# Performance work log

Measured on AMD Instinct MI355X. Metric: run time of the kernel, lower is better.

The kernel has to match this reference:

```python
import jax, jax.numpy as jnp
import numpy as np

DECAY = 0.8
COMMITMENT = 1.0
EPS = 1e-05


def setup_inputs() -> dict:
    key = jax.random.key(0)
    k1, k2 = jax.random.split(key)
    x = jax.random.normal(k1, (8, 4096, 256), dtype=jnp.float32)
    embed = jax.random.normal(k2, (8192, 256), dtype=jnp.float32)
    cluster_size = jnp.zeros((8192,), dtype=jnp.float32)
    embed_avg = embed  # torch registers embed_avg = embed.clone()
    return {"x": x, "embed": embed, "cluster_size": cluster_size, "embed_avg": embed_avg}


def reference(x, embed, cluster_size, embed_avg):
    # EuclideanCodebook.forward (training mode) + VectorQuantize straight-through.
    K, D = embed.shape
    shape = x.shape
    flatten = x.reshape(-1, D)  # [T, D], T = B*N

    dist = (2.0 * (flatten @ embed.T)
            - jnp.sum(flatten * flatten, axis=-1, keepdims=True)
            - jnp.sum(embed * embed, axis=-1)[None, :])  # [T, K]
    embed_ind = jnp.argmax(dist, axis=-1)  # [T]

    quantize = embed[embed_ind].reshape(shape)  # gather

    # EMA codebook statistics (scatter-add instead of materializing one-hot [T,K])
    bins = jax.ops.segment_sum(jnp.ones_like(embed_ind, dtype=x.dtype), embed_ind, num_segments=K)  # [K]
    embed_sum = jax.ops.segment_sum(flatten, embed_ind, num_segments=K)  # [K, D]

    new_cluster_size = cluster_size * DECAY + (1.0 - DECAY) * bins
    new_embed_avg = embed_avg * DECAY + (1.0 - DECAY) * embed_sum

    total = new_cluster_size.sum()
    smoothed = (new_cluster_size + EPS) / (total + K * EPS) * total  # laplace smoothing
    new_embed = new_embed_avg / smoothed[:, None]

    commit_loss = jnp.mean((jax.lax.stop_gradient(quantize) - x) ** 2) * COMMITMENT
    quantize_st = x + jax.lax.stop_gradient(quantize - x)  # straight-through

    ind_out = embed_ind.reshape(shape[:-1])
    return quantize_st, ind_out, commit_loss, new_embed, new_cluster_size, new_embed_avg
```

## Files before the change

kernel.cpp:

```cpp
#include <hip/hip_runtime.h>

#define DECAYF 0.8f
#define OMDF   0.2f
#define EPSF   1e-5f
#define COMMITF 1.0f
#define MARGINF 0.024f
#define FIXCAP  8192
#define MAXR    64

typedef _Float16 h8v __attribute__((ext_vector_type(8)));
typedef float f4v __attribute__((ext_vector_type(4)));

__device__ inline void gload_lds16(const void* g, void* l) {
  __builtin_amdgcn_global_load_lds(
      (const __attribute__((address_space(1))) unsigned int*)g,
      (__attribute__((address_space(3))) unsigned int*)l, 16, 0, 0);
}

__global__ __launch_bounds__(256) void k_pre(
    const float* __restrict__ embed, char* __restrict__ Ews,
    float* __restrict__ zero_p, int zero_n, float* __restrict__ ee, int K, int D)
{
  const int tid = threadIdx.x;
  const int gid0 = blockIdx.x * 256 + tid;
  const int gstride = gridDim.x * 256;

  for (int i = gid0; i < zero_n; i += gstride) zero_p[i] = 0.0f;

  for (int gid = gid0; gid < K * (D / 8); gid += gstride) {
    int k = gid >> 5;
    int d0 = (gid & 31) * 8;
    const float* ep = embed + (size_t)k * D + d0;
    float4 v0 = *(const float4*)(ep);
    float4 v1 = *(const float4*)(ep + 4);
    float f[8] = {v0.x, v0.y, v0.z, v0.w, v1.x, v1.y, v1.z, v1.w};
    h8v h;
#pragma unroll
    for (int e = 0; e < 8; ++e) h[e] = (_Float16)f[e];
    int tt = k >> 6;
    int c = k & 63;
    int byteoff = c * 512 + ((d0 * 2) ^ ((c & 7) << 4));
    *(h8v*)(Ews + (size_t)tt * 32768 + byteoff) = h;
  }

  {
    int wave = tid >> 6;
    int lane = tid & 63;
    int k = blockIdx.x * 4 + wave;
    if (k < K) {
      const float* e = embed + (size_t)k * D;
      float s = 0.f;
      for (int d = lane * 4; d < D; d += 256) {
        float4 v = *reinterpret_cast<const float4*>(e + d);
        s += v.x * v.x + v.y * v.y + v.z * v.z + v.w * v.w;
      }
      for (int off = 32; off > 0; off >>= 1) s += __shfl_down(s, off);
      if (lane == 0) ee[k] = 0.5f * s;
    }
  }
}

__device__ __forceinline__ void upd2(float s, int code, float& b1, float& b2, int& bi) {
  if (s > b1) { b2 = b1; b1 = s; bi = code; }
  else if (s > b2) { b2 = s; }
}

__device__ __forceinline__ void k_body(
    int TT, int NT, char* lds, const char* Ews, const float* ee,
    int w, int lane, int l15, int rowbyte0,
    const int (&dbyte)[8],
    const h8v (&xh)[4][8],
    f4v (&CUR)[4], f4v (&PRV)[4],
    float EEP, float& EEC,
    float (&best)[4][4], float (&bst2)[4][4], int (&bidx)[4][4])
{
  const int k0 = TT * 64;
  const char* cb = lds + (TT & 1) * 32768;
  if (TT + 1 < NT) {
    const char* src = Ews + (size_t)(TT + 1) * 32768 + w * 8192 + lane * 16;
    char* dst = lds + ((TT + 1) & 1) * 32768 + w * 8192;
#pragma unroll
    for (int q = 0; q < 8; ++q) gload_lds16(src + q * 1024, dst + q * 1024);
  }
  EEC = ee[k0 + w * 16 + l15];
  const int cp = k0 - 64 + w * 16 + l15;
#pragma unroll
  for (int rf = 0; rf < 4; ++rf) CUR[rf] = (f4v){0.f, 0.f, 0.f, 0.f};
  h8v B[2];
  B[0] = *(const h8v*)(cb + rowbyte0 + dbyte[0]);
#pragma unroll
  for (int ks = 0; ks < 8; ++ks) {
    const int cs = ks & 1, ns = cs ^ 1;
    if (ks < 7) B[ns] = *(const h8v*)(cb + rowbyte0 + dbyte[ks + 1]);
    __builtin_amdgcn_s_setprio(1);
    CUR[0] = __builtin_amdgcn_mfma_f32_16x16x32_f16(xh[0][ks], B[cs], CUR[0], 0, 0, 0);
    CUR[1] = __builtin_amdgcn_mfma_f32_16x16x32_f16(xh[1][ks], B[cs], CUR[1], 0, 0, 0);
    CUR[2] = __builtin_amdgcn_mfma_f32_16x16x32_f16(xh[2][ks], B[cs], CUR[2], 0, 0, 0);
    CUR[3] = __builtin_amdgcn_mfma_f32_16x16x32_f16(xh[3][ks], B[cs], CUR[3], 0, 0, 0);
    __builtin_amdgcn_s_setprio(0);
    {
      const int s0 = 2 * ks, s1 = 2 * ks + 1;
      const int rf0 = s0 >> 2, ii0 = s0 & 3;
      const int rf1 = s1 >> 2, ii1 = s1 & 3;
      upd2(PRV[rf0][ii0] - EEP, cp, best[rf0][ii0], bst2[rf0][ii0], bidx[rf0][ii0]);
      upd2(PRV[rf1][ii1] - EEP, cp, best[rf1][ii1], bst2[rf1][ii1], bidx[rf1][ii1]);
    }
  }
  __syncthreads();
}

__global__ __launch_bounds__(256, 2) void k_dist(
    const float* __restrict__ x, const char* __restrict__ Ews,
    const float* __restrict__ ee, float* __restrict__ ind_f,
    int* __restrict__ idx_out, int* __restrict__ wl, int* __restrict__ cnt,
    int T, int K)
{
  extern __shared__ char lds[];
  const int tid = threadIdx.x;
  const int w = tid >> 6, lane = tid & 63;
  const int l15 = lane & 15, lk = lane >> 4;
  const int row0 = blockIdx.x * 64;
  const int NT = K / 64;

  h8v xh[4][8];
#pragma unroll
  for (int rf = 0; rf < 4; ++rf) {
    const float* xp = x + (size_t)(row0 + rf * 16 + l15) * 256 + lk * 8;
#pragma unroll
    for (int ks = 0; ks < 8; ++ks) {
      float4 v0 = *(const float4*)(xp + ks * 32);
      float4 v1 = *(const float4*)(xp + ks * 32 + 4);
      float f[8] = {v0.x, v0.y, v0.z, v0.w, v1.x, v1.y, v1.z, v1.w};
      h8v h;
#pragma unroll
      for (int e = 0; e < 8; ++e) h[e] = (_Float16)f[e];
      xh[rf][ks] = h;
    }
  }

  float best[4][4], bst2[4][4];
  int bidx[4][4];
#pragma unroll
  for (int rf = 0; rf < 4; ++rf)
#pragma unroll
    for (int i = 0; i < 4; ++i) { best[rf][i] = -3.0e38f; bst2[rf][i] = -3.0e38f; bidx[rf][i] = 0; }

  const int swz = (l15 & 7) << 4;
  const int rowbyte0 = (w * 16 + l15) * 512;
  int dbyte[8];
#pragma unroll
  for (int ks = 0; ks < 8; ++ks) dbyte[ks] = (ks * 64 + lk * 16) ^ swz;

  {
    const char* src = Ews + (size_t)w * 8192 + lane * 16;
    char* dst = lds + w * 8192;
#pragma unroll
    for (int q = 0; q < 8; ++q)
      gload_lds16(src + q * 1024, dst + q * 1024);
  }
  __syncthreads();

  f4v accA[4], accB[4];
#pragma unroll
  for (int rf = 0; rf < 4; ++rf)
    accB[rf] = (f4v){-3.0e38f, -3.0e38f, -3.0e38f, -3.0e38f};
  float eeX = 0.f, eeY = 0.f;

  for (int tt = 0; tt < NT; tt += 2) {
    k_body(tt,     NT, lds, Ews, ee, w, lane, l15, rowbyte0, dbyte, xh,
           accA, accB, eeX, eeY, best, bst2, bidx);
    k_body(tt + 1, NT, lds, Ews, ee, w, lane, l15, rowbyte0, dbyte, xh,
           accB, accA, eeY, eeX, best, bst2, bidx);
  }
  {
    const int cp = (NT - 1) * 64 + w * 16 + l15;
#pragma unroll
    for (int rf = 0; rf < 4; ++rf)
#pragma unroll
      for (int ii = 0; ii < 4; ++ii)
        upd2(accB[rf][ii] - eeX, cp, best[rf][ii], bst2[rf][ii], bidx[rf][ii]);
  }

#pragma unroll
  for (int rf = 0; rf < 4; ++rf)
#pragma unroll
    for (int i = 0; i < 4; ++i) {
      float s = best[rf][i], s2 = bst2[rf][i];
      int mi = bidx[rf][i];
#pragma unroll
      for (int off = 1; off < 16; off <<= 1) {
        float os = __shfl_xor(s, off);
        float os2 = __shfl_xor(s2, off);
        int oi = __shfl_xor(mi, off);
        if (os > s || (os == s && oi < mi)) {
          s2 = fmaxf(s, os2);
          s = os; mi = oi;
        } else {
          s2 = fmaxf(s2, os);
        }
      }
      best[rf][i] = s; bst2[rf][i] = s2; bidx[rf][i] = mi;
    }

  float* S  = (float*)lds;
  float* S2 = S + 256;
  int*   MI = (int*)(S2 + 256);
  if (l15 == 0) {
#pragma unroll
    for (int rf = 0; rf < 4; ++rf)
#pragma unroll
      for (int i = 0; i < 4; ++i) {
        int rl = rf * 16 + lk * 4 + i;
        int a = w * 64 + rl;
        S[a]  = best[rf][i];
        S2[a] = bst2[rf][i];
        MI[a] = bidx[rf][i];
      }
  }
  __syncthreads();
  if (w == 0) {
    int r = lane;
    float s = S[r], s2 = S2[r];
    int mi = MI[r];
#pragma unroll
    for (int q = 1; q < 4; ++q) {
      float sq = S[q * 64 + r], s2q = S2[q * 64 + r];
      int miq = MI[q * 64 + r];
      if (sq > s) { s2 = fmaxf(s, s2q); s = sq; mi = miq; }
      else        { s2 = fmaxf(s2, sq); }
    }
    int row = row0 + r;
    idx_out[row] = mi;
    ind_f[row] = (float)mi;
    if (s - s2 < MARGINF) {
      int slot = atomicAdd(cnt, 1);
      if (slot < FIXCAP) wl[slot] = row;
    }
  }
}

__global__ __launch_bounds__(256) void k_fix1(
    const float* __restrict__ x, const float* __restrict__ embed,
    const float* __restrict__ ee, const int* __restrict__ wl,
    const int* __restrict__ cnt, float* __restrict__ pval,
    int* __restrict__ pidx)
{
  __shared__ float Xs[8][256];
  const int b = blockIdx.x & 255;
  const int g = blockIdx.x >> 8;
  const int t = threadIdx.x;
  int n = *cnt; if (n > FIXCAP) n = FIXCAP;
  const int c = b * 32 + (t & 31);
  const float* er = embed + (size_t)c * 256;
  const float eec = ee[c];
  const int rl = t >> 5;

  for (int r0 = g * 8; r0 < n; r0 += 32) {
    __syncthreads();
    for (int i = t; i < 8 * 64; i += 256) {
      int rr = i >> 6, dq = i & 63;
      int wi = r0 + rr; if (wi >= n) wi = n - 1;
      int row = wl[wi];
      ((float4*)Xs[rr])[dq] = *(const float4*)(x + (size_t)row * 256 + dq * 4);
    }
    __syncthreads();
    const float* xr = Xs[rl];
    float s0 = 0.f, s1 = 0.f, s2a = 0.f, s3 = 0.f;
#pragma unroll
    for (int d = 0; d < 256; d += 16) {
      float4 e0 = *(const float4*)(er + d);
      float4 e1 = *(const float4*)(er + d + 4);
      float4 e2 = *(const float4*)(er + d + 8);
      float4 e3 = *(const float4*)(er + d + 12);
      s0 = fmaf(xr[d + 0], e0.x, s0);  s0 = fmaf(xr[d + 1], e0.y, s0);
      s0 = fmaf(xr[d + 2], e0.z, s0);  s0 = fmaf(xr[d + 3], e0.w, s0);
      s1 = fmaf(xr[d + 4], e1.x, s1);  s1 = fmaf(xr[d + 5], e1.y, s1);
      s1 = fmaf(xr[d + 6], e1.z, s1);  s1 = fmaf(xr[d + 7], e1.w, s1);
      s2a = fmaf(xr[d + 8], e2.x, s2a);  s2a = fmaf(xr[d + 9], e2.y, s2a);
      s2a = fmaf(xr[d + 10], e2.z, s2a); s2a = fmaf(xr[d + 11], e2.w, s2a);
      s3 = fmaf(xr[d + 12], e3.x, s3);  s3 = fmaf(xr[d + 13], e3.y, s3);
      s3 = fmaf(xr[d + 14], e3.z, s3);  s3 = fmaf(xr[d + 15], e3.w, s3);
    }
    float s = ((s0 + s1) + (s2a + s3)) - eec;
    int mi = c;
#pragma unroll
    for (int off = 1; off < 32; off <<= 1) {
      float os = __shfl_xor(s, off);
      int oi = __shfl_xor(mi, off);
      if (os > s || (os == s && oi < mi)) { s = os; mi = oi; }
    }
    int wi = r0 + rl;
    if ((t & 31) == 0 && wi < n) {
      pval[(size_t)wi * 256 + b] = s;
      pidx[(size_t)wi * 256 + b] = mi;
    }
  }
}

__global__ __launch_bounds__(256) void k_fix2(
    const int* __restrict__ wl, const int* __restrict__ cnt,
    const float* __restrict__ pval, const int* __restrict__ pidx,
    float* __restrict__ ind_f, int* __restrict__ idx_out)
{
  __shared__ float bv[256];
  __shared__ int bi[256];
  const int t = threadIdx.x;
  int n = *cnt; if (n > FIXCAP) n = FIXCAP;
  for (int it = blockIdx.x; it < n; it += gridDim.x) {
    __syncthreads();
    bv[t] = pval[(size_t)it * 256 + t];
    bi[t] = pidx[(size_t)it * 256 + t];
    __syncthreads();
    for (int sh = 128; sh > 0; sh >>= 1) {
      if (t < sh) {
        if (bv[t + sh] > bv[t] || (bv[t + sh] == bv[t] && bi[t + sh] < bi[t])) {
          bv[t] = bv[t + sh]; bi[t] = bi[t + sh];
        }
      }
      __syncthreads();
    }
    if (t == 0) {
      int row = wl[it];
      idx_out[row] = bi[0];
      ind_f[row] = (float)bi[0];
    }
  }
}

__global__ __launch_bounds__(256) void k_cnt(
    const int* __restrict__ idx, int* __restrict__ cntr, int* __restrict__ rlist,
    int* __restrict__ olist, int* __restrict__ ocnt, int T)
{
  int r = blockIdx.x * 256 + threadIdx.x;
  if (r >= T) return;
  int k = idx[r];
  int slot = atomicAdd(&cntr[k], 1);
  if (slot < MAXR) rlist[k * MAXR + slot] = r;
  else { int o = atomicAdd(ocnt, 1); olist[o] = r; }
}

__global__ __launch_bounds__(256) void k_ovf(
    const float* __restrict__ x, const int* __restrict__ idx,
    const int* __restrict__ olist, const int* __restrict__ ocnt,
    float* __restrict__ ovfsum)
{
  int wave = threadIdx.x >> 6, lane = threadIdx.x & 63;
  int n = *ocnt;
  for (int i = blockIdx.x * 4 + wave; i < n; i += gridDim.x * 4) {
    int row = olist[i];
    int k = idx[row];
    int d0 = lane * 4;
    float4 xv = *(const float4*)(x + (size_t)row * 256 + d0);
    atomicAdd(&ovfsum[(size_t)k * 256 + d0 + 0], xv.x);
    atomicAdd(&ovfsum[(size_t)k * 256 + d0 + 1], xv.y);
    atomicAdd(&ovfsum[(size_t)k * 256 + d0 + 2], xv.z);
    atomicAdd(&ovfsum[(size_t)k * 256 + d0 + 3], xv.w);
  }
}

__global__ void k_gather(const float* __restrict__ x, const float* __restrict__ embed,
                         const int* __restrict__ idx, float* __restrict__ quant,
                         float* __restrict__ lslots, int T, int D)
{
  int wave = threadIdx.x >> 6;
  int lane = threadIdx.x & 63;
  int row = blockIdx.x * 4 + wave;
  if (row >= T) return;
  int k = idx[row];
  const float* xr = x + (size_t)row * D;
  const float* er = embed + (size_t)k * D;
  float* qr = quant + (size_t)row * D;
  float lsum = 0.f;
  for (int d = lane * 4; d < D; d += 256) {
    float4 xv = *reinterpret_cast<const float4*>(xr + d);
    float4 ev = *reinterpret_cast<const float4*>(er + d);
    *reinterpret_cast<float4*>(qr + d) = ev;
    float dx = ev.x - xv.x, dy = ev.y - xv.y, dz = ev.z - xv.z, dw = ev.w - xv.w;
    lsum += dx * dx + dy * dy + dz * dz + dw * dw;
  }
  for (int off = 32; off > 0; off >>= 1) lsum += __shfl_down(lsum, off);
  if (lane == 0) atomicAdd(&lslots[row & 255], lsum);
}

__global__ void k_ema1(const float* __restrict__ cs, const int* __restrict__ cntr,
                       float* __restrict__ ncs, float* __restrict__ total_acc, int K)
{
  int k = blockIdx.x * 256 + threadIdx.x;
  float v = 0.f;
  if (k < K) {
    v = cs[k] * DECAYF + OMDF * (float)cntr[k];
    ncs[k] = v;
  }
  for (int off = 32; off > 0; off >>= 1) v += __shfl_down(v, off);
  __shared__ float s4[4];
  if ((threadIdx.x & 63) == 0) s4[threadIdx.x >> 6] = v;
  __syncthreads();
  if (threadIdx.x == 0) atomicAdd(total_acc, s4[0] + s4[1] + s4[2] + s4[3]);
}

__global__ __launch_bounds__(256) void k_ema2(
    const float* __restrict__ x, const float* __restrict__ ea,
    const int* __restrict__ cntr, const int* __restrict__ rlist,
    const float* __restrict__ ovfsum, const float* __restrict__ ncs,
    const float* __restrict__ total_acc, float* __restrict__ ne,
    float* __restrict__ nea, int K, int D)
{
  int wave = threadIdx.x >> 6, lane = threadIdx.x & 63;
  int k = blockIdx.x * 4 + wave;
  if (k >= K) return;
  int c = cntr[k];
  int m = c < MAXR ? c : MAXR;
  int d0 = lane * 4;
  float4 s = *(const float4*)(ovfsum + (size_t)k * 256 + d0);
  for (int i = 0; i < m; ++i) {
    int r = rlist[k * MAXR + i];
    float4 xv = *(const float4*)(x + (size_t)r * 256 + d0);
    s.x += xv.x; s.y += xv.y; s.z += xv.z; s.w += xv.w;
  }
  float4 eav = *(const float4*)(ea + (size_t)k * 256 + d0);
  float total = *total_acc;
  float csk = ncs[k];
  float sm = (csk + EPSF) / (total + (float)K * EPSF) * total;
  float rs = 1.0f / sm;
  float v0 = eav.x * DECAYF + OMDF * s.x;
  float v1 = eav.y * DECAYF + OMDF * s.y;
  float v2 = eav.z * DECAYF + OMDF * s.z;
  float v3 = eav.w * DECAYF + OMDF * s.w;
  size_t o = (size_t)k * 256 + d0;
  nea[o + 0] = v0; nea[o + 1] = v1; nea[o + 2] = v2; nea[o + 3] = v3;
  ne[o + 0] = v0 * rs; ne[o + 1] = v1 * rs; ne[o + 2] = v2 * rs; ne[o + 3] = v3 * rs;
}

__global__ void k_loss(const float* __restrict__ lslots, float* __restrict__ out_loss,
                       float scale)
{
  int tid = threadIdx.x;
  float v = lslots[tid];
  for (int off = 32; off > 0; off >>= 1) v += __shfl_down(v, off);
  __shared__ float s4[4];
  if ((tid & 63) == 0) s4[tid >> 6] = v;
  __syncthreads();
  if (tid == 0) out_loss[0] = (s4[0] + s4[1] + s4[2] + s4[3]) * scale;
}

extern "C" void kernel_launch(void* const* d_in, const int* in_sizes, int n_in,
                              void* d_out, int out_size, void* d_ws, size_t ws_size,
                              hipStream_t stream)
{
  const float* x     = (const float*)d_in[0];
  const float* embed = (const float*)d_in[1];
  const float* cs    = (const float*)d_in[2];
  const float* ea    = (const float*)d_in[3];
  const int K = in_sizes[2];
  const int D = in_sizes[1] / K;
  const int T = in_sizes[0] / D;

  float* out   = (float*)d_out;
  float* o_q   = out;
  float* o_ind = out + (size_t)T * D;
  float* o_ls  = o_ind + T;
  float* o_ne  = o_ls + 1;
  float* o_ncs = o_ne + (size_t)K * D;
  float* o_nea = o_ncs + K;

  float* w      = (float*)d_ws;
  float* ee     = w;
  int*   idx    = (int*)(w + K);
  int*   wl     = idx + T;
  float* pval   = (float*)(wl + FIXCAP);
  int*   pidx   = (int*)(pval + (size_t)FIXCAP * 256);
  int*   rlist  = pidx + (size_t)FIXCAP * 256;
  int*   olist  = rlist + (size_t)K * MAXR;
  float* ovfsum = (float*)(olist + T);
  float* lslots = ovfsum + (size_t)K * D;
  float* total  = lslots + 256;
  int*   cnt    = (int*)(total + 1);
  int*   cntr   = cnt + 1;
  int*   ocnt   = cntr + K;
  int zero_n = K * D + 256 + 1 + 1 + K + 1;
  size_t ews_off = (((size_t)(ocnt + 1 - (int*)w)) + 63) & ~(size_t)63;
  char* Ews = (char*)(w + ews_off);

  k_pre<<<2048, 256, 0, stream>>>(embed, Ews, ovfsum, zero_n, ee, K, D);
  k_dist<<<T / 64, 256, 65536, stream>>>(x, Ews, ee, o_ind, idx, wl, cnt, T, K);
  k_fix1<<<1024, 256, 0, stream>>>(x, embed, ee, wl, cnt, pval, pidx);
  k_fix2<<<1024, 256, 0, stream>>>(wl, cnt, pval, pidx, o_ind, idx);
  k_cnt<<<(T + 255) / 256, 256, 0, stream>>>(idx, cntr, rlist, olist, ocnt, T);
  k_ovf<<<128, 256, 0, stream>>>(x, idx, olist, ocnt, ovfsum);
  k_gather<<<(T + 3) / 4, 256, 0, stream>>>(x, embed, idx, o_q, lslots, T, D);
  k_ema1<<<(K + 255) / 256, 256, 0, stream>>>(cs, cntr, o_ncs, total, K);
  k_ema2<<<(K + 3) / 4, 256, 0, stream>>>(x, ea, cntr, rlist, ovfsum, o_ncs, total,
                                          o_ne, o_nea, K, D);
  k_loss<<<1, 256, 0, stream>>>(lslots, o_ls, COMMITF / ((float)T * (float)D));
}
```

Measured before the change: 476.7 us.

## Fuse gather, loss and bin counting into distance and fix kernels

Moves the codeword gather, commitment-loss accumulation and per-code row-list bucketing into the tail of the distance kernel for rows that are confidently assigned. Rows flagged for exact re-check are handled the same way at the end of the fix2 kernel once their final index is known. This drops two separate kernel launches and a re-read of the index array. In exchange the distance kernel gets a longer serial epilogue with atomics, and the LDS allocation becomes static.

```diff
diff --git a/kernel.cpp b/kernel.cpp
--- a/kernel.cpp
+++ b/kernel.cpp
@@ -111,11 +111,15 @@
 
 __global__ __launch_bounds__(256, 2) void k_dist(
     const float* __restrict__ x, const char* __restrict__ Ews,
-    const float* __restrict__ ee, float* __restrict__ ind_f,
-    int* __restrict__ idx_out, int* __restrict__ wl, int* __restrict__ cnt,
+    const float* __restrict__ ee, const float* __restrict__ embed,
+    float* __restrict__ ind_f, int* __restrict__ idx_out,
+    int* __restrict__ wl, int* __restrict__ cnt,
+    float* __restrict__ quant, float* __restrict__ lslots,
+    int* __restrict__ cntr, int* __restrict__ rlist,
+    int* __restrict__ olist, int* __restrict__ ocnt,
     int T, int K)
 {
-  extern __shared__ char lds[];
+  __shared__ char lds[65536];
   const int tid = threadIdx.x;
   const int w = tid >> 6, lane = tid & 63;
   const int l15 = lane & 15, lk = lane >> 4;
@@ -205,6 +209,8 @@
   float* S  = (float*)lds;
   float* S2 = S + 256;
   int*   MI = (int*)(S2 + 256);
+  int*   FK = MI + 256;
+  int*   FF = FK + 64;
   if (l15 == 0) {
 #pragma unroll
     for (int rf = 0; rf < 4; ++rf)
@@ -232,9 +238,31 @@
     int row = row0 + r;
     idx_out[row] = mi;
     ind_f[row] = (float)mi;
+    int flagged = 0;
     if (s - s2 < MARGINF) {
       int slot = atomicAdd(cnt, 1);
-      if (slot < FIXCAP) wl[slot] = row;
+      if (slot < FIXCAP) { wl[slot] = row; flagged = 1; }
+    }
+    FK[r] = mi;
+    FF[r] = flagged;
+  }
+  __syncthreads();
+
+  for (int rr = w * 16; rr < w * 16 + 16; ++rr) {
+    if (FF[rr]) continue;
+    const int row = row0 + rr;
+    const int k = FK[rr];
+    const float4 xv = *(const float4*)(x + (size_t)row * 256 + lane * 4);
+    const float4 ev = *(const float4*)(embed + (size_t)k * 256 + lane * 4);
+    *(float4*)(quant + (size_t)row * 256 + lane * 4) = ev;
+    float dx = ev.x - xv.x, dy = ev.y - xv.y, dz = ev.z - xv.z, dw = ev.w - xv.w;
+    float l = dx * dx + dy * dy + dz * dz + dw * dw;
+    for (int off = 32; off > 0; off >>= 1) l += __shfl_down(l, off);
+    if (lane == 0) {
+      atomicAdd(&lslots[row & 255], l);
+      int slot = atomicAdd(&cntr[k], 1);
+      if (slot < MAXR) rlist[k * MAXR + slot] = row;
+      else { int o = atomicAdd(ocnt, 1); olist[o] = row; }
     }
   }
 }
@@ -298,9 +326,13 @@
 }
 
 __global__ __launch_bounds__(256) void k_fix2(
+    const float* __restrict__ x, const float* __restrict__ embed,
     const int* __restrict__ wl, const int* __restrict__ cnt,
     const float* __restrict__ pval, const int* __restrict__ pidx,
-    float* __restrict__ ind_f, int* __restrict__ idx_out)
+    float* __restrict__ ind_f, int* __restrict__ idx_out,
+    float* __restrict__ quant, float* __restrict__ lslots,
+    int* __restrict__ cntr, int* __restrict__ rlist,
+    int* __restrict__ olist, int* __restrict__ ocnt)
 {
   __shared__ float bv[256];
   __shared__ int bi[256];
@@ -319,24 +351,28 @@
       }
       __syncthreads();
     }
+    const int row = wl[it];
+    const int kf = bi[0];
     if (t == 0) {
-      int row = wl[it];
-      idx_out[row] = bi[0];
-      ind_f[row] = (float)bi[0];
-    }
-  }
-}
-
-__global__ __launch_bounds__(256) void k_cnt(
-    const int* __restrict__ idx, int* __restrict__ cntr, int* __restrict__ rlist,
-    int* __restrict__ olist, int* __restrict__ ocnt, int T)
-{
-  int r = blockIdx.x * 256 + threadIdx.x;
-  if (r >= T) return;
-  int k = idx[r];
-  int slot = atomicAdd(&cntr[k], 1);
-  if (slot < MAXR) rlist[k * MAXR + slot] = r;
-  else { int o = atomicAdd(ocnt, 1); olist[o] = r; }
+      idx_out[row] = kf;
+      ind_f[row] = (float)kf;
+      int slot = atomicAdd(&cntr[kf], 1);
+      if (slot < MAXR) rlist[kf * MAXR + slot] = row;
+      else { int o = atomicAdd(ocnt, 1); olist[o] = row; }
+    }
+    float xv = x[(size_t)row * 256 + t];
+    float ev = embed[(size_t)kf * 256 + t];
+    quant[(size_t)row * 256 + t] = ev;
+    float d = ev - xv;
+    __syncthreads();
+    bv[t] = d * d;
+    __syncthreads();
+    for (int sh = 128; sh > 0; sh >>= 1) {
+      if (t < sh) bv[t] += bv[t + sh];
+      __syncthreads();
+    }
+    if (t == 0) atomicAdd(&lslots[row & 255], bv[0]);
+  }
 }
 
 __global__ __launch_bounds__(256) void k_ovf(
@@ -356,30 +392,6 @@
     atomicAdd(&ovfsum[(size_t)k * 256 + d0 + 2], xv.z);
     atomicAdd(&ovfsum[(size_t)k * 256 + d0 + 3], xv.w);
   }
-}
-
-__global__ void k_gather(const float* __restrict__ x, const float* __restrict__ embed,
-                         const int* __restrict__ idx, float* __restrict__ quant,
-                         float* __restrict__ lslots, int T, int D)
-{
-  int wave = threadIdx.x >> 6;
-  int lane = threadIdx.x & 63;
-  int row = blockIdx.x * 4 + wave;
-  if (row >= T) return;
-  int k = idx[row];
-  const float* xr = x + (size_t)row * D;
-  const float* er = embed + (size_t)k * D;
-  float* qr = quant + (size_t)row * D;
-  float lsum = 0.f;
-  for (int d = lane * 4; d < D; d += 256) {
-    float4 xv = *reinterpret_cast<const float4*>(xr + d);
-    float4 ev = *reinterpret_cast<const float4*>(er + d);
-    *reinterpret_cast<float4*>(qr + d) = ev;
-    float dx = ev.x - xv.x, dy = ev.y - xv.y, dz = ev.z - xv.z, dw = ev.w - xv.w;
-    lsum += dx * dx + dy * dy + dz * dz + dw * dw;
-  }
-  for (int off = 32; off > 0; off >>= 1) lsum += __shfl_down(lsum, off);
-  if (lane == 0) atomicAdd(&lslots[row & 255], lsum);
 }
 
 __global__ void k_ema1(const float* __restrict__ cs, const int* __restrict__ cntr,
@@ -482,12 +494,12 @@
   char* Ews = (char*)(w + ews_off);
 
   k_pre<<<2048, 256, 0, stream>>>(embed, Ews, ovfsum, zero_n, ee, K, D);
-  k_dist<<<T / 64, 256, 65536, stream>>>(x, Ews, ee, o_ind, idx, wl, cnt, T, K);
+  k_dist<<<T / 64, 256, 0, stream>>>(x, Ews, ee, embed, o_ind, idx, wl, cnt,
+                                     o_q, lslots, cntr, rlist, olist, ocnt, T, K);
   k_fix1<<<1024, 256, 0, stream>>>(x, embed, ee, wl, cnt, pval, pidx);
-  k_fix2<<<1024, 256, 0, stream>>>(wl, cnt, pval, pidx, o_ind, idx);
-  k_cnt<<<(T + 255) / 256, 256, 0, stream>>>(idx, cntr, rlist, olist, ocnt, T);
+  k_fix2<<<1024, 256, 0, stream>>>(x, embed, wl, cnt, pval, pidx, o_ind, idx,
+                                   o_q, lslots, cntr, rlist, olist, ocnt);
   k_ovf<<<128, 256, 0, stream>>>(x, idx, olist, ocnt, ovfsum);
-  k_gather<<<(T + 3) / 4, 256, 0, stream>>>(x, embed, idx, o_q, lslots, T, D);
   k_ema1<<<(K + 255) / 256, 256, 0, stream>>>(cs, cntr, o_ncs, total, K);
   k_ema2<<<(K + 3) / 4, 256, 0, stream>>>(x, ea, cntr, rlist, ovfsum, o_ncs, total,
                                           o_ne, o_nea, K, D);
```

Result: no change. 467.6 us (-1.9%).
